# Performance work log

Measured on AMD Instinct MI355X. Metric: run time of the kernel, lower is better.

## Reference

```python
import jax, jax.numpy as jnp
from jax import lax
import numpy as np

T, B, I, H, O = 512, 64, 256, 512, 128

def _rnn_dir(x, h0, Wih, Whh, bih, bhh, reverse):
    # x: (T,B,in), Wih: (H,in), Whh: (H,H)
    xw = jnp.einsum('tbi,hi->tbh', x, Wih) + bih + bhh  # precompute input proj + both biases
    def step(h, xt):
        h = jnp.tanh(xt + h @ Whh.T)
        return h, h
    hT, ys = lax.scan(step, h0, xw, reverse=reverse)
    # with reverse=True, ys[t] is the backward hidden state at original time t (PyTorch layout)
    return ys, hT

def _bidir_layer(x, h0f, h0b, pf, pb):
    yf, hTf = _rnn_dir(x, h0f, pf[0], pf[1], pf[2], pf[3], False)
    yb, hTb = _rnn_dir(x, h0b, pb[0], pb[1], pb[2], pb[3], True)
    return jnp.concatenate([yf, yb], axis=-1), hTf, hTb

def setup_inputs() -> dict:
    key = jax.random.key(0)
    ks = jax.random.split(key, 24)
    s = 1.0 / np.sqrt(H)
    def u(k, shape):
        return jax.random.uniform(k, shape, jnp.float32, -s, s)
    inp = {
        'x': jax.random.normal(ks[0], (T, B, I), jnp.float32),
        'h_0': jax.random.normal(ks[1], (4, B, H), jnp.float32),
        # layer 0 forward / backward (input size I)
        'Wih_l0f': u(ks[2], (H, I)), 'Whh_l0f': u(ks[3], (H, H)), 'bih_l0f': u(ks[4], (H,)), 'bhh_l0f': u(ks[5], (H,)),
        'Wih_l0b': u(ks[6], (H, I)), 'Whh_l0b': u(ks[7], (H, H)), 'bih_l0b': u(ks[8], (H,)), 'bhh_l0b': u(ks[9], (H,)),
        # layer 1 forward / backward (input size 2H)
        'Wih_l1f': u(ks[10], (H, 2 * H)), 'Whh_l1f': u(ks[11], (H, H)), 'bih_l1f': u(ks[12], (H,)), 'bhh_l1f': u(ks[13], (H,)),
        'Wih_l1b': u(ks[14], (H, 2 * H)), 'Whh_l1b': u(ks[15], (H, H)), 'bih_l1b': u(ks[16], (H,)), 'bhh_l1b': u(ks[17], (H,)),
        # FC head
        'Wfc': u(ks[18], (O, 2 * H)), 'bfc': u(ks[19], (O,)),
    }
    return inp

def reference(x, h_0, Wih_l0f, Whh_l0f, bih_l0f, bhh_l0f, Wih_l0b, Whh_l0b, bih_l0b, bhh_l0b,
              Wih_l1f, Whh_l1f, bih_l1f, bhh_l1f, Wih_l1b, Whh_l1b, bih_l1b, bhh_l1b, Wfc, bfc):
    y0, hTf0, hTb0 = _bidir_layer(x, h_0[0], h_0[1],
                                  (Wih_l0f, Whh_l0f, bih_l0f, bhh_l0f),
                                  (Wih_l0b, Whh_l0b, bih_l0b, bhh_l0b))
    y1, hTf1, hTb1 = _bidir_layer(y0, h_0[2], h_0[3],
                                  (Wih_l1f, Whh_l1f, bih_l1f, bhh_l1f),
                                  (Wih_l1b, Whh_l1b, bih_l1b, bhh_l1b))
    h_T = jnp.stack([hTf0, hTb0, hTf1, hTb1])  # (4,B,H), PyTorch layer-major, dir-minor order
    logits = jnp.einsum('tbh,oh->tbo', y1, Wfc) + bfc
    probs = jax.nn.softmax(logits, axis=2)
    return probs, h_T
```

## Files before the change

kernel.cpp:

```cpp
#include <hip/hip_runtime.h>


#define T_ 512
#define B_ 64
#define I_ 256
#define H_ 512
#define O_ 128

typedef short  bf16x8 __attribute__((ext_vector_type(8)));
typedef float  f32x4  __attribute__((ext_vector_type(4)));

__device__ __forceinline__ unsigned short bf_hi(float x){
  unsigned u = __float_as_uint(x);
  unsigned r = u + 0x7fffu + ((u>>16)&1u);
  return (unsigned short)(r>>16);
}
__device__ __forceinline__ float bf_f(unsigned short h){ return __uint_as_float(((unsigned)h)<<16); }

__device__ __forceinline__ uint4 pack_quad(float4 v){
  unsigned short h0=bf_hi(v.x), h1=bf_hi(v.y), h2=bf_hi(v.z), h3=bf_hi(v.w);
  unsigned short l0=bf_hi(v.x-bf_f(h0)), l1=bf_hi(v.y-bf_f(h1)),
                 l2=bf_hi(v.z-bf_f(h2)), l3=bf_hi(v.w-bf_f(h3));
  uint4 r;
  r.x = (unsigned)h0 | ((unsigned)h1<<16);
  r.y = (unsigned)h2 | ((unsigned)h3<<16);
  r.z = (unsigned)l0 | ((unsigned)l1<<16);
  r.w = (unsigned)l2 | ((unsigned)l3<<16);
  return r;
}

__device__ __forceinline__ void frag_from_quads(const unsigned char* p0, const unsigned char* p1,
                                                bf16x8& hi, bf16x8& lo){
  bf16x8 a = *reinterpret_cast<const bf16x8*>(p0);
  bf16x8 b = *reinterpret_cast<const bf16x8*>(p1);
  hi = __builtin_shufflevector(a,b, 0,1,2,3, 8,9,10,11);
  lo = __builtin_shufflevector(a,b, 4,5,6,7, 12,13,14,15);
}

__global__ __launch_bounds__(256,2)
void gemm_bt(const float* __restrict__ X, const float* __restrict__ W,
             const float* __restrict__ b1, const float* __restrict__ b2,
             float* __restrict__ C, int M, int N, int K)
{
  __shared__ __align__(16) unsigned char lds[32768];
  const int t = threadIdx.x, lane = t&63, w = t>>6;
  const int wm = w>>1, wn = w&1;
  const int mb = blockIdx.x<<7, nb = blockIdx.y<<7;
  const int nk = K>>5, kf4 = K>>2;
  const float4* Xf4 = reinterpret_cast<const float4*>(X);
  const float4* Wf4 = reinterpret_cast<const float4*>(W);

  f32x4 acc[4][4];
  #pragma unroll
  for(int i=0;i<4;i++)
    #pragma unroll
    for(int j=0;j<4;j++) acc[i][j] = (f32x4){0.f,0.f,0.f,0.f};

  float4 ra[4], rb[4];
  #pragma unroll
  for(int c=0;c<4;c++){
    int idx=(c<<8)+t, row=idx>>3, kq=idx&7;
    ra[c] = Xf4[(size_t)(mb+row)*kf4 + kq];
    rb[c] = Wf4[(size_t)(nb+row)*kf4 + kq];
  }

  for(int kb=0; kb<nk; kb++){
    #pragma unroll
    for(int c=0;c<4;c++){
      int idx=(c<<8)+t, row=idx>>3, kq=idx&7;
      int swz = (row&7)<<4;
      *reinterpret_cast<uint4*>(lds +         row*128 + ((kq<<4)^swz)) = pack_quad(ra[c]);
      *reinterpret_cast<uint4*>(lds + 16384 + row*128 + ((kq<<4)^swz)) = pack_quad(rb[c]);
    }
    __syncthreads();
    if(kb+1<nk){
      #pragma unroll
      for(int c=0;c<4;c++){
        int idx=(c<<8)+t, row=idx>>3, kq=idx&7;
        ra[c] = Xf4[(size_t)(mb+row)*kf4 + (size_t)(kb+1)*8 + kq];
        rb[c] = Wf4[(size_t)(nb+row)*kf4 + (size_t)(kb+1)*8 + kq];
      }
    }
    bf16x8 ah[4],al[4],bh[4],bl[4];
    const int q0 = (lane>>4)<<1;
    #pragma unroll
    for(int i=0;i<4;i++){
      int rowA = (wm<<6) + (i<<4) + (lane&15); int sa=(rowA&7)<<4;
      frag_from_quads(lds + rowA*128 + ((q0<<4)^sa),
                      lds + rowA*128 + (((q0+1)<<4)^sa), ah[i], al[i]);
      int rowB = (wn<<6) + (i<<4) + (lane&15); int sb=(rowB&7)<<4;
      frag_from_quads(lds + 16384 + rowB*128 + ((q0<<4)^sb),
                      lds + 16384 + rowB*128 + (((q0+1)<<4)^sb), bh[i], bl[i]);
    }
    #pragma unroll
    for(int i=0;i<4;i++)
      #pragma unroll
      for(int j=0;j<4;j++){
        acc[i][j] = __builtin_amdgcn_mfma_f32_16x16x32_bf16(ah[i], bh[j], acc[i][j], 0,0,0);
        acc[i][j] = __builtin_amdgcn_mfma_f32_16x16x32_bf16(ah[i], bl[j], acc[i][j], 0,0,0);
        acc[i][j] = __builtin_amdgcn_mfma_f32_16x16x32_bf16(al[i], bh[j], acc[i][j], 0,0,0);
      }
    __syncthreads();
  }

  #pragma unroll
  for(int j=0;j<4;j++){
    int col = nb + (wn<<6) + (j<<4) + (lane&15);
    float bs = (b1?b1[col]:0.f) + (b2?b2[col]:0.f);
    #pragma unroll
    for(int i=0;i<4;i++){
      int r0 = mb + (wm<<6) + (i<<4) + ((lane>>4)<<2);
      #pragma unroll
      for(int r=0;r<4;r++)
        C[(size_t)(r0+r)*N + col] = acc[i][j][r] + bs;
    }
  }
}

__global__ __launch_bounds__(256,1)
void rnn_scan(const float* __restrict__ xw_f, const float* __restrict__ xw_b,
              const float* __restrict__ Whh_f, const float* __restrict__ Whh_b,
              const float* __restrict__ h0base,
              float* __restrict__ y,
              float* __restrict__ hT,
              unsigned int* __restrict__ flags)
{
  __shared__ __align__(16) unsigned char lds[163840];
  const int t = threadIdx.x, lane = t&63, w = t>>6;
  const int bid = blockIdx.x;
  const int dir = bid>>5, mg = (bid>>3)&3, js = bid&7;
  const float* xw  = dir ? xw_b : xw_f;
  const float* Whh = dir ? Whh_b : Whh_f;
  const float* h0  = h0base + (size_t)dir*B_*H_;
  unsigned int* flag = flags + (dir*4 + mg)*64;

  {
    const float4* Wf4 = reinterpret_cast<const float4*>(Whh);
    #pragma unroll
    for(int c=0;c<32;c++){
      int idx=(c<<8)+t, row=idx>>7, q=idx&127;
      float4 v = Wf4[(size_t)((js<<6)+row)*(H_>>2) + q];
      int swz=(row&7)<<4;
      *reinterpret_cast<uint4*>(lds + (row<<11) + ((q<<4)^swz)) = pack_quad(v);
    }
  }
  __syncthreads();

  const int jg   = (js<<6) + (w<<4) + (lane&15);
  const int ml0  = (lane>>4)<<2;
  const int mg16 = mg<<4;

  for(int step=0; step<T_; step++){
    const int tt  = dir ? (T_-1-step) : step;
    const int ttp = dir ? (tt+1) : (tt-1);

    float xv[4];
    #pragma unroll
    for(int r=0;r<4;r++)
      xv[r] = xw[((size_t)tt*B_ + mg16 + ml0 + r)*H_ + jg];

    if(step>0 && t==0){
      unsigned target = 8u*(unsigned)step;
      int guard = 0;
      while(__hip_atomic_load(flag, __ATOMIC_RELAXED, __HIP_MEMORY_SCOPE_AGENT) < target
            && ++guard < 400000)
        __builtin_amdgcn_s_sleep(1);
    }
    __syncthreads();
    asm volatile("" ::: "memory");

    if(step==0){
      #pragma unroll
      for(int c=0;c<8;c++){
        int idx=(c<<8)+t, row=idx>>7, q=idx&127;
        float4 v = reinterpret_cast<const float4*>(h0)[(size_t)(mg16+row)*(H_>>2) + q];
        int swz=(row&7)<<4;
        *reinterpret_cast<uint4*>(lds + 131072 + (row<<11) + ((q<<4)^swz)) = pack_quad(v);
      }
    } else {
      unsigned long long u[16];
      #pragma unroll
      for(int c=0;c<8;c++){
        int idx=(c<<8)+t, row=idx>>7, q=idx&127;
        const unsigned long long* srcq = reinterpret_cast<const unsigned long long*>(
            y + ((size_t)ttp*B_ + mg16+row)*(2*H_) + dir*H_) + (q<<1);
        u[2*c  ] = __hip_atomic_load(srcq,   __ATOMIC_RELAXED, __HIP_MEMORY_SCOPE_AGENT);
        u[2*c+1] = __hip_atomic_load(srcq+1, __ATOMIC_RELAXED, __HIP_MEMORY_SCOPE_AGENT);
      }
      #pragma unroll
      for(int c=0;c<8;c++){
        int idx=(c<<8)+t, row=idx>>7, q=idx&127;
        float4 v;
        v.x = __uint_as_float((unsigned)(u[2*c  ] & 0xffffffffu));
        v.y = __uint_as_float((unsigned)(u[2*c  ] >> 32));
        v.z = __uint_as_float((unsigned)(u[2*c+1] & 0xffffffffu));
        v.w = __uint_as_float((unsigned)(u[2*c+1] >> 32));
        int swz=(row&7)<<4;
        *reinterpret_cast<uint4*>(lds + 131072 + (row<<11) + ((q<<4)^swz)) = pack_quad(v);
      }
    }
    __syncthreads();

    f32x4 a0={0.f,0.f,0.f,0.f}, a1=a0, a2=a0;
    #pragma unroll
    for(int kk=0; kk<16; kk++){
      int rowA = lane&15, sa=(rowA&7)<<4;
      int qa = (kk<<3) + ((lane>>4)<<1);
      bf16x8 ah, alo;
      frag_from_quads(lds + 131072 + (rowA<<11) + ((qa<<4)^sa),
                      lds + 131072 + (rowA<<11) + (((qa+1)<<4)^sa), ah, alo);
      int rowB = (w<<4) + (lane&15), sb=(rowB&7)<<4;
      int qb = (kk<<3) + ((lane>>4)<<1);
      bf16x8 bh, bl;
      frag_from_quads(lds + (rowB<<11) + ((qb<<4)^sb),
                      lds + (rowB<<11) + (((qb+1)<<4)^sb), bh, bl);
      a0 = __builtin_amdgcn_mfma_f32_16x16x32_bf16(ah,  bh, a0, 0,0,0);
      a1 = __builtin_amdgcn_mfma_f32_16x16x32_bf16(ah,  bl, a1, 0,0,0);
      a2 = __builtin_amdgcn_mfma_f32_16x16x32_bf16(alo, bh, a2, 0,0,0);
    }

    float hv[4];
    #pragma unroll
    for(int r=0;r<4;r++){
      float z = a0[r]+a1[r]+a2[r] + xv[r];
      z = fminf(fmaxf(z,-15.f),15.f);
      float e = __expf(2.f*z);
      hv[r] = (e-1.f)/(e+1.f);
    }
    #pragma unroll
    for(int r=0;r<4;r++){
      __hip_atomic_store(y + ((size_t)tt*B_ + mg16+ml0+r)*(2*H_) + dir*H_ + jg, hv[r],
                         __ATOMIC_RELAXED, __HIP_MEMORY_SCOPE_AGENT);
    }
    if(step==T_-1){
      #pragma unroll
      for(int r=0;r<4;r++)
        hT[(size_t)dir*B_*H_ + (size_t)(mg16+ml0+r)*H_ + jg] = hv[r];
    }
    asm volatile("s_waitcnt vmcnt(0)" ::: "memory");
    __syncthreads();
    if(t==0) __hip_atomic_fetch_add(flag, 1u, __ATOMIC_RELAXED, __HIP_MEMORY_SCOPE_AGENT);
  }
}

__global__ __launch_bounds__(256)
void softmax_rows(float* __restrict__ P){
  const int row = (blockIdx.x<<2) + (threadIdx.x>>6);
  const int l = threadIdx.x & 63;
  float2* p = reinterpret_cast<float2*>(P) + (size_t)row*(O_/2) + l;
  float2 v = *p;
  float m = fmaxf(v.x, v.y);
  #pragma unroll
  for(int off=32; off; off>>=1) m = fmaxf(m, __shfl_xor(m, off, 64));
  float e0 = __expf(v.x-m), e1 = __expf(v.y-m);
  float s = e0+e1;
  #pragma unroll
  for(int off=32; off; off>>=1) s += __shfl_xor(s, off, 64);
  float inv = 1.f/s;
  *p = make_float2(e0*inv, e1*inv);
}

extern "C" void kernel_launch(void* const* d_in, const int* in_sizes, int n_in,
                              void* d_out, int out_size, void* d_ws, size_t ws_size,
                              hipStream_t stream)
{
  (void)in_sizes; (void)n_in; (void)out_size; (void)ws_size;
  const float* x     = (const float*)d_in[0];
  const float* h0    = (const float*)d_in[1];
  const float* Wih0f = (const float*)d_in[2];
  const float* Whh0f = (const float*)d_in[3];
  const float* bih0f = (const float*)d_in[4];
  const float* bhh0f = (const float*)d_in[5];
  const float* Wih0b = (const float*)d_in[6];
  const float* Whh0b = (const float*)d_in[7];
  const float* bih0b = (const float*)d_in[8];
  const float* bhh0b = (const float*)d_in[9];
  const float* Wih1f = (const float*)d_in[10];
  const float* Whh1f = (const float*)d_in[11];
  const float* bih1f = (const float*)d_in[12];
  const float* bhh1f = (const float*)d_in[13];
  const float* Wih1b = (const float*)d_in[14];
  const float* Whh1b = (const float*)d_in[15];
  const float* bih1b = (const float*)d_in[16];
  const float* bhh1b = (const float*)d_in[17];
  const float* Wfc   = (const float*)d_in[18];
  const float* bfc   = (const float*)d_in[19];

  const size_t MR = (size_t)T_*B_;
  float* xwF  = (float*)d_ws;
  float* xwB  = xwF + MR*H_;
  float* bufA = xwF + 2*MR*H_;
  float* probs = (float*)d_out;
  float* hTout = probs + MR*O_;
  unsigned int* flags = (unsigned int*)d_out;

  hipMemsetAsync(flags, 0, 8192, stream);

  dim3 blk(256);
  gemm_bt<<<dim3(MR/128, H_/128), blk, 0, stream>>>(x, Wih0f, bih0f, bhh0f, xwF, (int)MR, H_, I_);
  gemm_bt<<<dim3(MR/128, H_/128), blk, 0, stream>>>(x, Wih0b, bih0b, bhh0b, xwB, (int)MR, H_, I_);
  rnn_scan<<<64, blk, 0, stream>>>(xwF, xwB, Whh0f, Whh0b, h0, bufA, hTout, flags);
  gemm_bt<<<dim3(MR/128, H_/128), blk, 0, stream>>>(bufA, Wih1f, bih1f, bhh1f, xwF, (int)MR, H_, 2*H_);
  gemm_bt<<<dim3(MR/128, H_/128), blk, 0, stream>>>(bufA, Wih1b, bih1b, bhh1b, xwB, (int)MR, H_, 2*H_);
  rnn_scan<<<64, blk, 0, stream>>>(xwF, xwB, Whh1f, Whh1b, h0 + 2*B_*H_, bufA, hTout + 2*B_*H_, flags + 512);
  gemm_bt<<<dim3(MR/128, 1), blk, 0, stream>>>(bufA, Wfc, bfc, nullptr, probs, (int)MR, O_, 2*H_);
  softmax_rows<<<MR/4, blk, 0, stream>>>(probs);
}
```

Before: 4.140 ms.

## Replace per-step flag counters with sentinel polling on hidden-state data

Removes the atomic flag counter, the spin-wait on it and the end-of-step waitcnt, barrier and fetch_add in the recurrent scan. Each block now polls the previous step's hidden-state values directly until all are nonzero. Every stored h has its low mantissa bit forced to 1, so a written value can never look like an unwritten zero. The output buffer is zeroed with a large memset before each scan. This cuts one global round-trip and a barrier from the per-step critical path. In exchange it adds two full-buffer memsets and a one-ulp perturbation of every hidden value.

Result: slower. 4.714 ms (+13.9%).

```diff
diff --git a/kernel.cpp b/kernel.cpp
--- a/kernel.cpp
+++ b/kernel.cpp
@@ -122,8 +122,7 @@
               const float* __restrict__ Whh_f, const float* __restrict__ Whh_b,
               const float* __restrict__ h0base,
               float* __restrict__ y,
-              float* __restrict__ hT,
-              unsigned int* __restrict__ flags)
+              float* __restrict__ hT)
 {
   __shared__ __align__(16) unsigned char lds[163840];
   const int t = threadIdx.x, lane = t&63, w = t>>6;
@@ -132,7 +131,6 @@
   const float* xw  = dir ? xw_b : xw_f;
   const float* Whh = dir ? Whh_b : Whh_f;
   const float* h0  = h0base + (size_t)dir*B_*H_;
-  unsigned int* flag = flags + (dir*4 + mg)*64;
 
   {
     const float4* Wf4 = reinterpret_cast<const float4*>(Whh);
@@ -159,15 +157,7 @@
     for(int r=0;r<4;r++)
       xv[r] = xw[((size_t)tt*B_ + mg16 + ml0 + r)*H_ + jg];
 
-    if(step>0 && t==0){
-      unsigned target = 8u*(unsigned)step;
-      int guard = 0;
-      while(__hip_atomic_load(flag, __ATOMIC_RELAXED, __HIP_MEMORY_SCOPE_AGENT) < target
-            && ++guard < 400000)
-        __builtin_amdgcn_s_sleep(1);
-    }
     __syncthreads();
-    asm volatile("" ::: "memory");
 
     if(step==0){
       #pragma unroll
@@ -178,15 +168,29 @@
         *reinterpret_cast<uint4*>(lds + 131072 + (row<<11) + ((q<<4)^swz)) = pack_quad(v);
       }
     } else {
-      unsigned long long u[16];
+      const unsigned long long* srcs[8];
       #pragma unroll
       for(int c=0;c<8;c++){
         int idx=(c<<8)+t, row=idx>>7, q=idx&127;
-        const unsigned long long* srcq = reinterpret_cast<const unsigned long long*>(
+        srcs[c] = reinterpret_cast<const unsigned long long*>(
             y + ((size_t)ttp*B_ + mg16+row)*(2*H_) + dir*H_) + (q<<1);
-        u[2*c  ] = __hip_atomic_load(srcq,   __ATOMIC_RELAXED, __HIP_MEMORY_SCOPE_AGENT);
-        u[2*c+1] = __hip_atomic_load(srcq+1, __ATOMIC_RELAXED, __HIP_MEMORY_SCOPE_AGENT);
-      }
+      }
+      unsigned long long u[16];
+      unsigned done = 0;
+      int guard = 0;
+      do{
+        #pragma unroll
+        for(int c=0;c<8;c++) if(!(done&(1u<<c))){
+          u[2*c  ] = __hip_atomic_load(srcs[c],   __ATOMIC_RELAXED, __HIP_MEMORY_SCOPE_AGENT);
+          u[2*c+1] = __hip_atomic_load(srcs[c]+1, __ATOMIC_RELAXED, __HIP_MEMORY_SCOPE_AGENT);
+        }
+        #pragma unroll
+        for(int c=0;c<8;c++) if(!(done&(1u<<c))){
+          if((unsigned)(u[2*c  ]&0xffffffffu) && (unsigned)(u[2*c  ]>>32) &&
+             (unsigned)(u[2*c+1]&0xffffffffu) && (unsigned)(u[2*c+1]>>32))
+            done |= 1u<<c;
+        }
+      } while(done != 0xffu && ++guard < 20000);
       #pragma unroll
       for(int c=0;c<8;c++){
         int idx=(c<<8)+t, row=idx>>7, q=idx&127;
@@ -225,7 +229,8 @@
       float z = a0[r]+a1[r]+a2[r] + xv[r];
       z = fminf(fmaxf(z,-15.f),15.f);
       float e = __expf(2.f*z);
-      hv[r] = (e-1.f)/(e+1.f);
+      float h = (e-1.f)/(e+1.f);
+      hv[r] = __uint_as_float(__float_as_uint(h) | 1u);
     }
     #pragma unroll
     for(int r=0;r<4;r++){
@@ -237,9 +242,6 @@
       for(int r=0;r<4;r++)
         hT[(size_t)dir*B_*H_ + (size_t)(mg16+ml0+r)*H_ + jg] = hv[r];
     }
-    asm volatile("s_waitcnt vmcnt(0)" ::: "memory");
-    __syncthreads();
-    if(t==0) __hip_atomic_fetch_add(flag, 1u, __ATOMIC_RELAXED, __HIP_MEMORY_SCOPE_AGENT);
   }
 }
 
@@ -292,17 +294,17 @@
   float* bufA = xwF + 2*MR*H_;
   float* probs = (float*)d_out;
   float* hTout = probs + MR*O_;
-  unsigned int* flags = (unsigned int*)d_out;
-
-  hipMemsetAsync(flags, 0, 8192, stream);
+  const size_t YBYTES = MR*2*H_*sizeof(float);
 
   dim3 blk(256);
+  hipMemsetAsync(bufA, 0, YBYTES, stream);
   gemm_bt<<<dim3(MR/128, H_/128), blk, 0, stream>>>(x, Wih0f, bih0f, bhh0f, xwF, (int)MR, H_, I_);
   gemm_bt<<<dim3(MR/128, H_/128), blk, 0, stream>>>(x, Wih0b, bih0b, bhh0b, xwB, (int)MR, H_, I_);
-  rnn_scan<<<64, blk, 0, stream>>>(xwF, xwB, Whh0f, Whh0b, h0, bufA, hTout, flags);
+  rnn_scan<<<64, blk, 0, stream>>>(xwF, xwB, Whh0f, Whh0b, h0, bufA, hTout);
   gemm_bt<<<dim3(MR/128, H_/128), blk, 0, stream>>>(bufA, Wih1f, bih1f, bhh1f, xwF, (int)MR, H_, 2*H_);
   gemm_bt<<<dim3(MR/128, H_/128), blk, 0, stream>>>(bufA, Wih1b, bih1b, bhh1b, xwB, (int)MR, H_, 2*H_);
-  rnn_scan<<<64, blk, 0, stream>>>(xwF, xwB, Whh1f, Whh1b, h0 + 2*B_*H_, bufA, hTout + 2*B_*H_, flags + 512);
+  hipMemsetAsync(bufA, 0, YBYTES, stream);
+  rnn_scan<<<64, blk, 0, stream>>>(xwF, xwB, Whh1f, Whh1b, h0 + 2*B_*H_, bufA, hTout + 2*B_*H_);
   gemm_bt<<<dim3(MR/128, 1), blk, 0, stream>>>(bufA, Wfc, bfc, nullptr, probs, (int)MR, O_, 2*H_);
   softmax_rows<<<MR/4, blk, 0, stream>>>(probs);
 }
```
